# Kernel optimization log

Measured on AMD Instinct MI355X. Metric: run time of the kernel, lower is better.

The kernel has to match this reference:

```python
import jax, jax.numpy as jnp
import numpy as np

N_NODES = 100000
N_EDGES = 1600000
D_IN = 64
D_EDGE = 64
D_OUT = 64


def setup_inputs() -> dict:
    key = jax.random.key(0)
    ks = jax.random.split(key, 8)
    nfeats = jax.random.normal(ks[0], (N_NODES, 1, D_IN), dtype=jnp.float32)
    efeats = jax.random.normal(ks[1], (N_EDGES, 1, D_EDGE), dtype=jnp.float32)
    src = jax.random.randint(ks[2], (N_EDGES,), 0, N_NODES, dtype=jnp.int32)
    dst = jax.random.randint(ks[3], (N_EDGES,), 0, N_NODES, dtype=jnp.int32)
    # Linear weights stored torch-style as [out, in]
    W_msg_w = jax.random.normal(ks[4], (D_OUT, D_IN + D_EDGE), dtype=jnp.float32) * 0.05
    W_msg_b = jax.random.normal(ks[5], (D_OUT,), dtype=jnp.float32) * 0.05
    W_apply_w = jax.random.normal(ks[6], (D_OUT, D_IN + D_OUT), dtype=jnp.float32) * 0.05
    W_apply_b = jax.random.normal(ks[7], (D_OUT,), dtype=jnp.float32) * 0.05
    return {"nfeats": nfeats, "efeats": efeats, "src": src, "dst": dst,
            "W_msg_w": W_msg_w, "W_msg_b": W_msg_b,
            "W_apply_w": W_apply_w, "W_apply_b": W_apply_b}


def reference(nfeats, efeats, src, dst, W_msg_w, W_msg_b, W_apply_w, W_apply_b):
    n_nodes = nfeats.shape[0]
    h = nfeats[:, 0, :]          # [N, D_IN]
    e = efeats[:, 0, :]          # [E, D_EDGE]
    # message: per-edge gather of src node feats, concat with edge feats, linear
    src_h = h[src]               # [E, D_IN]
    msg = jnp.concatenate([src_h, e], axis=1) @ W_msg_w.T + W_msg_b  # [E, D_OUT]
    # mean aggregation over incoming edges per destination node
    msg_sum = jax.ops.segment_sum(msg, dst, num_segments=n_nodes)    # [N, D_OUT]
    deg = jax.ops.segment_sum(jnp.ones((msg.shape[0],), msg.dtype), dst,
                              num_segments=n_nodes)                  # [N]
    h_neigh = jnp.where(deg[:, None] > 0, msg_sum / jnp.maximum(deg, 1.0)[:, None], 0.0)
    # apply: concat self + neighborhood, linear, activation
    combined = jnp.concatenate([h, h_neigh], axis=1) @ W_apply_w.T + W_apply_b
    out = jax.nn.relu(combined)[:, None, :]  # [N, 1, D_OUT]
    return out
```

## Files before the change

### kernel.cpp

```cpp
#include <hip/hip_runtime.h>

#define N_NODES 100000
#define N_EDGES 1600000
#define NB_SCAN 49

typedef __attribute__((ext_vector_type(8))) short bf16x8;
typedef __attribute__((ext_vector_type(4))) float f32x4;


__global__ void k_zero(int* __restrict__ p, int n) {
    int i = blockIdx.x * blockDim.x + threadIdx.x;
    if (i < n) p[i] = 0;
}

__global__ void k_count(const int* __restrict__ dst, int* __restrict__ cnt) {
    int e = blockIdx.x * blockDim.x + threadIdx.x;
    if (e < N_EDGES) atomicAdd(&cnt[dst[e]], 1);
}

__global__ void k_partial(const int* __restrict__ cnt, int* __restrict__ part) {
    __shared__ int red[256];
    int t = threadIdx.x;
    int base = blockIdx.x * 2048 + t * 8;
    int s = 0;
    if (base < N_NODES) {
        const int4* p = (const int4*)(cnt + base);
        int4 a = p[0], b = p[1];
        s = a.x + a.y + a.z + a.w + b.x + b.y + b.z + b.w;
    }
    red[t] = s;
    __syncthreads();
    for (int d = 128; d > 0; d >>= 1) {
        if (t < d) red[t] += red[t + d];
        __syncthreads();
    }
    if (t == 0) part[blockIdx.x] = red[0];
}

__global__ void k_scan_part(int* __restrict__ part, int nb) {
    int lane = threadIdx.x;
    int v = (lane < nb) ? part[lane] : 0;
    int incl = v;
    #pragma unroll
    for (int d = 1; d < 64; d <<= 1) {
        int u = __shfl_up(incl, d, 64);
        if (lane >= d) incl += u;
    }
    if (lane < nb) part[lane] = incl - v;
}

__global__ void k_scan_chunks(const int* __restrict__ cnt, const int* __restrict__ part,
                              int* __restrict__ off) {
    __shared__ int wtot[4];
    __shared__ int wexc[4];
    int t = threadIdx.x, b = blockIdx.x;
    int base = b * 2048 + t * 8;
    int4 a = {0, 0, 0, 0}, c = {0, 0, 0, 0};
    if (base < N_NODES) {
        const int4* p = (const int4*)(cnt + base);
        a = p[0];
        c = p[1];
    }
    int s0 = a.x, s1 = s0 + a.y, s2 = s1 + a.z, s3 = s2 + a.w;
    int s4 = s3 + c.x, s5 = s4 + c.y, s6 = s5 + c.z, s7 = s6 + c.w;
    int tot = s7;
    int lane = t & 63, wid = t >> 6;
    int incl = tot;
    #pragma unroll
    for (int d = 1; d < 64; d <<= 1) {
        int u = __shfl_up(incl, d, 64);
        if (lane >= d) incl += u;
    }
    if (lane == 63) wtot[wid] = incl;
    __syncthreads();
    if (t == 0) {
        int r = 0;
        for (int i = 0; i < 4; i++) { int v = wtot[i]; wexc[i] = r; r += v; }
    }
    __syncthreads();
    int texc = incl - tot + wexc[wid] + part[b];
    if (base < N_NODES) {
        int4 o0 = {texc, texc + s0, texc + s1, texc + s2};
        int4 o1 = {texc + s3, texc + s4, texc + s5, texc + s6};
        ((int4*)(off + base))[0] = o0;
        ((int4*)(off + base))[1] = o1;
    }
}

__global__ void k_scatter64(const int* __restrict__ dst, const int* __restrict__ src,
                            const int* __restrict__ off, int* __restrict__ cur,
                            unsigned long long* __restrict__ code64) {
    int e = blockIdx.x * blockDim.x + threadIdx.x;
    if (e < N_EDGES) {
        int d = dst[e];
        int p = off[d] + atomicAdd(&cur[d], 1);
        code64[p] = ((unsigned long long)(unsigned)src[e] << 32) | (unsigned)e;
    }
}

__global__ void k_scatter32(const int* __restrict__ dst, const int* __restrict__ off,
                            int* __restrict__ cur, int* __restrict__ eid) {
    int e = blockIdx.x * blockDim.x + threadIdx.x;
    if (e < N_EDGES) {
        int d = dst[e];
        int p = off[d] + atomicAdd(&cur[d], 1);
        eid[p] = e;
    }
}

__device__ __forceinline__ unsigned short f2bf(float f) {
    unsigned u = __float_as_uint(f);
    return (unsigned short)((u + 0x7FFFu + ((u >> 16) & 1u)) >> 16);
}

__global__ void k_prec(const float* __restrict__ Wm, const float* __restrict__ bm,
                       const float* __restrict__ Wa, const float* __restrict__ ba,
                       unsigned short* __restrict__ Wf, float* __restrict__ bc) {
    int o = blockIdx.x;
    int k = threadIdx.x;
    const float* war = Wa + o * 128 + 64;
    float w;
    if (k < 64) {
        w = Wa[o * 128 + k];
    } else {
        int m = k - 64;
        float s = 0.f;
        #pragma unroll 8
        for (int j = 0; j < 64; j++) s += war[j] * Wm[j * 128 + m];
        w = s;
    }
    Wf[o * 192 + k] = f2bf(w);
    if (k == 0) {
        float t = ba[o];
        for (int j = 0; j < 64; j++) t += war[j] * bm[j];
        bc[o] = t;
    }
}

__device__ __forceinline__ float4 ld_feat(const float* __restrict__ nf,
                                          const float* __restrict__ ef,
                                          unsigned long long c, int slot) {
    unsigned e = (unsigned)c;
    unsigned sv = (unsigned)(c >> 32);
    const float* p = (slot < 16) ? (nf + (size_t)sv * 64 + slot * 4)
                                 : (ef + (size_t)e * 64 + (slot - 16) * 4);
    return *(const float4*)p;
}

__global__ __launch_bounds__(256) void k_agg(
    const float* __restrict__ nf, const float* __restrict__ ef,
    const int* __restrict__ cnt, const int* __restrict__ off,
    const unsigned long long* __restrict__ code64, float* __restrict__ aggG) {
    int tid = threadIdx.x, lane = tid & 63, wid = tid >> 6;
    int n = blockIdx.x * 4 + wid;
    if (n >= N_NODES) return;
    int slot = lane & 31, half = lane >> 5;
    int st = off[n], deg = cnt[n];
    int pend = st + deg;
    float4 acc = make_float4(0.f, 0.f, 0.f, 0.f);
    int p = st + half;
    for (; p + 6 < pend; p += 8) {
        unsigned long long c0 = code64[p];
        unsigned long long c1 = code64[p + 2];
        unsigned long long c2 = code64[p + 4];
        unsigned long long c3 = code64[p + 6];
        float4 a0 = ld_feat(nf, ef, c0, slot);
        float4 a1 = ld_feat(nf, ef, c1, slot);
        float4 a2 = ld_feat(nf, ef, c2, slot);
        float4 a3 = ld_feat(nf, ef, c3, slot);
        acc.x += a0.x + a1.x + a2.x + a3.x;
        acc.y += a0.y + a1.y + a2.y + a3.y;
        acc.z += a0.z + a1.z + a2.z + a3.z;
        acc.w += a0.w + a1.w + a2.w + a3.w;
    }
    for (; p < pend; p += 2) {
        unsigned long long c = code64[p];
        float4 a = ld_feat(nf, ef, c, slot);
        acc.x += a.x; acc.y += a.y; acc.z += a.z; acc.w += a.w;
    }
    acc.x += __shfl_xor(acc.x, 32, 64);
    acc.y += __shfl_xor(acc.y, 32, 64);
    acc.z += __shfl_xor(acc.z, 32, 64);
    acc.w += __shfl_xor(acc.w, 32, 64);
    if (half == 0) {
        float inv = (deg > 0) ? 1.f / (float)deg : 0.f;
        acc.x *= inv; acc.y *= inv; acc.z *= inv; acc.w *= inv;
        *(float4*)(aggG + (size_t)n * 128 + slot * 4) = acc;
    }
}

__device__ __forceinline__ void st_bf4(unsigned short* p, float4 v) {
    unsigned lo = (unsigned)f2bf(v.x) | ((unsigned)f2bf(v.y) << 16);
    unsigned hi = (unsigned)f2bf(v.z) | ((unsigned)f2bf(v.w) << 16);
    uint2 u = {lo, hi};
    *(uint2*)p = u;
}

__global__ __launch_bounds__(256) void k_apply_mfma(
    const float* __restrict__ nf, const float* __restrict__ aggG,
    const int* __restrict__ cnt, const unsigned short* __restrict__ Wf,
    const float* __restrict__ ba, const float* __restrict__ bc,
    float* __restrict__ out) {
    __shared__ __align__(16) unsigned short cat[64][200];
    __shared__ __align__(16) unsigned short wt[64][200];
    __shared__ float degl[64];

    int tid = threadIdx.x;
    int base = blockIdx.x * 64;

    {
        const unsigned* Wfu = (const unsigned*)Wf;
        #pragma unroll
        for (int r = 0; r < 24; r++) {
            int u = r * 256 + tid;
            int o = u / 96;
            int c = u - o * 96;
            *(unsigned*)&wt[o][2 * c] = Wfu[u];
        }
    }
    {
        const float4* n4 = (const float4*)nf;
        #pragma unroll
        for (int r = 0; r < 4; r++) {
            int f = r * 256 + tid;
            int nl = f >> 4, c4 = f & 15;
            float4 v = make_float4(0.f, 0.f, 0.f, 0.f);
            if (base + nl < N_NODES) v = n4[(size_t)(base + nl) * 16 + c4];
            st_bf4(&cat[nl][c4 * 4], v);
        }
    }
    {
        const float4* g4 = (const float4*)aggG;
        #pragma unroll
        for (int r = 0; r < 8; r++) {
            int f = r * 256 + tid;
            int nl = f >> 5, c4 = f & 31;
            float4 v = make_float4(0.f, 0.f, 0.f, 0.f);
            if (base + nl < N_NODES) v = g4[(size_t)(base + nl) * 32 + c4];
            st_bf4(&cat[nl][64 + c4 * 4], v);
        }
    }
    if (tid < 64) degl[tid] = (base + tid < N_NODES) ? (float)cnt[base + tid] : 0.f;
    __syncthreads();

    int lane = tid & 63, w = tid >> 6;
    int sn = w * 16;
    int lr = lane & 15;
    int lg = lane >> 4;

    bf16x8 a[6];
    #pragma unroll
    for (int ks = 0; ks < 6; ks++)
        a[ks] = *(const bf16x8*)&cat[sn + lr][ks * 32 + lg * 8];

    float degv[4];
    #pragma unroll
    for (int r = 0; r < 4; r++) degv[r] = degl[sn + lg * 4 + r];

    #pragma unroll
    for (int cb = 0; cb < 4; cb++) {
        f32x4 acc = {0.f, 0.f, 0.f, 0.f};
        #pragma unroll
        for (int ks = 0; ks < 6; ks++) {
            bf16x8 b = *(const bf16x8*)&wt[cb * 16 + lr][ks * 32 + lg * 8];
            acc = __builtin_amdgcn_mfma_f32_16x16x32_bf16(a[ks], b, acc, 0, 0, 0);
        }
        int o = cb * 16 + lr;
        float bcv = bc[o], bav = ba[o];
        #pragma unroll
        for (int r = 0; r < 4; r++) {
            int n = base + sn + lg * 4 + r;
            if (n < N_NODES) {
                float v = acc[r] + ((degv[r] > 0.f) ? bcv : bav);
                out[(size_t)n * 64 + o] = fmaxf(v, 0.f);
            }
        }
    }
}

__global__ __launch_bounds__(256) void k_node_fb(
    const float* __restrict__ nf, const float* __restrict__ ef,
    const int* __restrict__ src, const int* __restrict__ cnt,
    const int* __restrict__ off, const int* __restrict__ eid,
    const float* __restrict__ Wm, const float* __restrict__ bm,
    const float* __restrict__ Wa, const float* __restrict__ ba,
    float* __restrict__ out) {
    __shared__ __align__(16) float agg[64][132];
    __shared__ __align__(16) float hn[64][68];
    __shared__ float degl[64];

    int tid = threadIdx.x, lane = tid & 63, wid = tid >> 6;
    int base = blockIdx.x * 64;

    for (int q = 0; q < 16; q++) {
        int nl = wid * 16 + q;
        int n = base + nl;
        float sh = 0.f, se = 0.f;
        int dg = 0;
        if (n < N_NODES) {
            dg = cnt[n];
            int st = off[n];
            for (int c0 = 0; c0 < dg; c0 += 64) {
                int m = dg - c0;
                if (m > 64) m = 64;
                int e_l = 0, s_l = 0;
                if (lane < m) {
                    e_l = eid[st + c0 + lane];
                    s_l = src[e_l];
                }
                for (int j = 0; j < m; j++) {
                    int e = __shfl(e_l, j, 64);
                    int s = __shfl(s_l, j, 64);
                    sh += nf[(size_t)s * 64 + lane];
                    se += ef[(size_t)e * 64 + lane];
                }
            }
        }
        agg[nl][lane] = sh;
        agg[nl][64 + lane] = se;
        if (lane == 0) degl[nl] = (float)dg;
    }
    __syncthreads();

    int og = (tid & 15) * 4;
    int ng = (tid >> 4) * 4;
    float acc[4][4] = {};
    const float4* Wm4 = (const float4*)Wm;
    #pragma unroll 4
    for (int k4 = 0; k4 < 32; k4++) {
        float4 av[4], wv[4];
        #pragma unroll
        for (int i = 0; i < 4; i++) av[i] = *(const float4*)&agg[ng + i][k4 * 4];
        #pragma unroll
        for (int j = 0; j < 4; j++) wv[j] = Wm4[(og + j) * 32 + k4];
        #pragma unroll
        for (int i = 0; i < 4; i++)
            #pragma unroll
            for (int j = 0; j < 4; j++)
                acc[i][j] += av[i].x * wv[j].x + av[i].y * wv[j].y +
                             av[i].z * wv[j].z + av[i].w * wv[j].w;
    }
    #pragma unroll
    for (int i = 0; i < 4; i++) {
        float d = degl[ng + i];
        float inv = (d > 0.f) ? 1.f / d : 0.f;
        #pragma unroll
        for (int j = 0; j < 4; j++) {
            float v = (d > 0.f) ? acc[i][j] * inv + bm[og + j] : 0.f;
            hn[ng + i][og + j] = v;
        }
    }
    __syncthreads();

    float acc2[4][4] = {};
    const float4* Wa4 = (const float4*)Wa;
    #pragma unroll 4
    for (int k4 = 0; k4 < 16; k4++) {
        float4 hv[4], wv[4];
        #pragma unroll
        for (int i = 0; i < 4; i++) {
            int n = base + ng + i;
            if (n < N_NODES)
                hv[i] = ((const float4*)(nf + (size_t)n * 64))[k4];
            else
                hv[i] = make_float4(0.f, 0.f, 0.f, 0.f);
        }
        #pragma unroll
        for (int j = 0; j < 4; j++) wv[j] = Wa4[(og + j) * 32 + k4];
        #pragma unroll
        for (int i = 0; i < 4; i++)
            #pragma unroll
            for (int j = 0; j < 4; j++)
                acc2[i][j] += hv[i].x * wv[j].x + hv[i].y * wv[j].y +
                              hv[i].z * wv[j].z + hv[i].w * wv[j].w;
    }
    #pragma unroll 4
    for (int k4 = 0; k4 < 16; k4++) {
        float4 hv[4], wv[4];
        #pragma unroll
        for (int i = 0; i < 4; i++) hv[i] = *(const float4*)&hn[ng + i][k4 * 4];
        #pragma unroll
        for (int j = 0; j < 4; j++) wv[j] = Wa4[(og + j) * 32 + 16 + k4];
        #pragma unroll
        for (int i = 0; i < 4; i++)
            #pragma unroll
            for (int j = 0; j < 4; j++)
                acc2[i][j] += hv[i].x * wv[j].x + hv[i].y * wv[j].y +
                              hv[i].z * wv[j].z + hv[i].w * wv[j].w;
    }
    #pragma unroll
    for (int i = 0; i < 4; i++) {
        int n = base + ng + i;
        if (n < N_NODES) {
            float4 o;
            o.x = fmaxf(acc2[i][0] + ba[og + 0], 0.f);
            o.y = fmaxf(acc2[i][1] + ba[og + 1], 0.f);
            o.z = fmaxf(acc2[i][2] + ba[og + 2], 0.f);
            o.w = fmaxf(acc2[i][3] + ba[og + 3], 0.f);
            *(float4*)&out[(size_t)n * 64 + og] = o;
        }
    }
}

extern "C" void kernel_launch(void* const* d_in, const int* in_sizes, int n_in,
                              void* d_out, int out_size, void* d_ws, size_t ws_size,
                              hipStream_t stream) {
    const float* nf = (const float*)d_in[0];
    const float* ef = (const float*)d_in[1];
    const int* src = (const int*)d_in[2];
    const int* dst = (const int*)d_in[3];
    const float* Wm = (const float*)d_in[4];
    const float* bm = (const float*)d_in[5];
    const float* Wa = (const float*)d_in[6];
    const float* ba = (const float*)d_in[7];
    float* out = (float*)d_out;

    int* cnt = (int*)d_ws;
    int* cur = cnt + N_NODES;
    int* part = cur + N_NODES;
    int* off = part + 64;
    size_t csr_bytes = (size_t)(3 * N_NODES + 64) * 4;

    int nz = 2 * N_NODES + 64;
    k_zero<<<(nz + 255) / 256, 256, 0, stream>>>(cnt, nz);
    k_count<<<(N_EDGES + 255) / 256, 256, 0, stream>>>(dst, cnt);
    k_partial<<<NB_SCAN, 256, 0, stream>>>(cnt, part);
    k_scan_part<<<1, 64, 0, stream>>>(part, NB_SCAN);
    k_scan_chunks<<<NB_SCAN, 256, 0, stream>>>(cnt, part, off);

    size_t need = csr_bytes + (size_t)N_EDGES * 8 + (size_t)N_NODES * 128 * 4 +
                  (size_t)64 * 192 * 2 + 512;
    if (ws_size >= need) {
        unsigned long long* code64 = (unsigned long long*)((char*)d_ws + csr_bytes);
        float* aggG = (float*)((char*)code64 + (size_t)N_EDGES * 8);
        unsigned short* Wf = (unsigned short*)(aggG + (size_t)N_NODES * 128);
        float* bc = (float*)(Wf + 64 * 192);
        k_prec<<<64, 192, 0, stream>>>(Wm, bm, Wa, ba, Wf, bc);
        k_scatter64<<<(N_EDGES + 255) / 256, 256, 0, stream>>>(dst, src, off, cur, code64);
        k_agg<<<N_NODES / 4, 256, 0, stream>>>(nf, ef, cnt, off, code64, aggG);
        k_apply_mfma<<<(N_NODES + 63) / 64, 256, 0, stream>>>(nf, aggG, cnt, Wf, ba, bc, out);
    } else {
        int* eid = (int*)((char*)d_ws + csr_bytes);
        k_scatter32<<<(N_EDGES + 255) / 256, 256, 0, stream>>>(dst, off, cur, eid);
        k_node_fb<<<(N_NODES + 63) / 64, 256, 0, stream>>>(nf, ef, src, cnt, off, eid,
                                                           Wm, bm, Wa, ba, out);
    }
}
```

Before: 315.9 us.

## Fuse edge aggregation and MFMA apply into one per-16-node kernel

Merges the gather/mean aggregation kernel and the MFMA apply kernel into a single 1024-thread block that aggregates 16 nodes (one wave each) into bf16 shared memory and then runs the 16x64 GEMM on four waves. This removes the fp32 aggG intermediate round-trip through global memory (about 51 MB of writes and reads) and one launch. In exchange, each block reloads the full weight tile into LDS for only 16 nodes, 12 of 16 waves sit idle during the MFMA phase, and the per-block barrier ties all waves to the slowest node's degree.

```diff
diff --git a/kernel.cpp b/kernel.cpp
--- a/kernel.cpp
+++ b/kernel.cpp
@@ -147,13 +147,39 @@
     return *(const float4*)p;
 }
 
-__global__ __launch_bounds__(256) void k_agg(
+__device__ __forceinline__ void st_bf4(unsigned short* p, float4 v) {
+    unsigned lo = (unsigned)f2bf(v.x) | ((unsigned)f2bf(v.y) << 16);
+    unsigned hi = (unsigned)f2bf(v.z) | ((unsigned)f2bf(v.w) << 16);
+    uint2 u = {lo, hi};
+    *(uint2*)p = u;
+}
+
+__global__ __launch_bounds__(1024) void k_fused(
     const float* __restrict__ nf, const float* __restrict__ ef,
     const int* __restrict__ cnt, const int* __restrict__ off,
-    const unsigned long long* __restrict__ code64, float* __restrict__ aggG) {
-    int tid = threadIdx.x, lane = tid & 63, wid = tid >> 6;
-    int n = blockIdx.x * 4 + wid;
-    if (n >= N_NODES) return;
+    const unsigned long long* __restrict__ code64,
+    const unsigned short* __restrict__ Wf,
+    const float* __restrict__ ba, const float* __restrict__ bc,
+    float* __restrict__ out) {
+    __shared__ __align__(16) unsigned short cat[16][200];
+    __shared__ __align__(16) unsigned short wt[64][200];
+    __shared__ float degl[16];
+
+    int tid = threadIdx.x, lane = tid & 63, w = tid >> 6;
+    int base = blockIdx.x * 16;
+    int n = base + w;
+
+    {
+        const unsigned* Wfu = (const unsigned*)Wf;
+        #pragma unroll
+        for (int r = 0; r < 6; r++) {
+            int u = r * 1024 + tid;
+            int o = u / 96;
+            int c = u - o * 96;
+            *(unsigned*)&wt[o][2 * c] = Wfu[u];
+        }
+    }
+
     int slot = lane & 31, half = lane >> 5;
     int st = off[n], deg = cnt[n];
     int pend = st + deg;
@@ -182,99 +208,42 @@
     acc.y += __shfl_xor(acc.y, 32, 64);
     acc.z += __shfl_xor(acc.z, 32, 64);
     acc.w += __shfl_xor(acc.w, 32, 64);
+
     if (half == 0) {
         float inv = (deg > 0) ? 1.f / (float)deg : 0.f;
         acc.x *= inv; acc.y *= inv; acc.z *= inv; acc.w *= inv;
-        *(float4*)(aggG + (size_t)n * 128 + slot * 4) = acc;
-    }
-}
-
-__device__ __forceinline__ void st_bf4(unsigned short* p, float4 v) {
-    unsigned lo = (unsigned)f2bf(v.x) | ((unsigned)f2bf(v.y) << 16);
-    unsigned hi = (unsigned)f2bf(v.z) | ((unsigned)f2bf(v.w) << 16);
-    uint2 u = {lo, hi};
-    *(uint2*)p = u;
-}
-
-__global__ __launch_bounds__(256) void k_apply_mfma(
-    const float* __restrict__ nf, const float* __restrict__ aggG,
-    const int* __restrict__ cnt, const unsigned short* __restrict__ Wf,
-    const float* __restrict__ ba, const float* __restrict__ bc,
-    float* __restrict__ out) {
-    __shared__ __align__(16) unsigned short cat[64][200];
-    __shared__ __align__(16) unsigned short wt[64][200];
-    __shared__ float degl[64];
-
-    int tid = threadIdx.x;
-    int base = blockIdx.x * 64;
-
-    {
-        const unsigned* Wfu = (const unsigned*)Wf;
-        #pragma unroll
-        for (int r = 0; r < 24; r++) {
-            int u = r * 256 + tid;
-            int o = u / 96;
-            int c = u - o * 96;
-            *(unsigned*)&wt[o][2 * c] = Wfu[u];
-        }
-    }
-    {
-        const float4* n4 = (const float4*)nf;
-        #pragma unroll
-        for (int r = 0; r < 4; r++) {
-            int f = r * 256 + tid;
-            int nl = f >> 4, c4 = f & 15;
-            float4 v = make_float4(0.f, 0.f, 0.f, 0.f);
-            if (base + nl < N_NODES) v = n4[(size_t)(base + nl) * 16 + c4];
-            st_bf4(&cat[nl][c4 * 4], v);
-        }
-    }
-    {
-        const float4* g4 = (const float4*)aggG;
-        #pragma unroll
-        for (int r = 0; r < 8; r++) {
-            int f = r * 256 + tid;
-            int nl = f >> 5, c4 = f & 31;
-            float4 v = make_float4(0.f, 0.f, 0.f, 0.f);
-            if (base + nl < N_NODES) v = g4[(size_t)(base + nl) * 32 + c4];
-            st_bf4(&cat[nl][64 + c4 * 4], v);
-        }
-    }
-    if (tid < 64) degl[tid] = (base + tid < N_NODES) ? (float)cnt[base + tid] : 0.f;
-    __syncthreads();
-
-    int lane = tid & 63, w = tid >> 6;
-    int sn = w * 16;
+        st_bf4(&cat[w][64 + slot * 4], acc);
+    } else if (slot < 16) {
+        float4 hv = ((const float4*)(nf + (size_t)n * 64))[slot];
+        st_bf4(&cat[w][slot * 4], hv);
+    }
+    if (lane == 0) degl[w] = (float)deg;
+    __syncthreads();
+
+    if (w >= 4) return;
+    int cb = w;
     int lr = lane & 15;
     int lg = lane >> 4;
 
     bf16x8 a[6];
     #pragma unroll
     for (int ks = 0; ks < 6; ks++)
-        a[ks] = *(const bf16x8*)&cat[sn + lr][ks * 32 + lg * 8];
-
-    float degv[4];
-    #pragma unroll
-    for (int r = 0; r < 4; r++) degv[r] = degl[sn + lg * 4 + r];
-
-    #pragma unroll
-    for (int cb = 0; cb < 4; cb++) {
-        f32x4 acc = {0.f, 0.f, 0.f, 0.f};
-        #pragma unroll
-        for (int ks = 0; ks < 6; ks++) {
-            bf16x8 b = *(const bf16x8*)&wt[cb * 16 + lr][ks * 32 + lg * 8];
-            acc = __builtin_amdgcn_mfma_f32_16x16x32_bf16(a[ks], b, acc, 0, 0, 0);
-        }
-        int o = cb * 16 + lr;
-        float bcv = bc[o], bav = ba[o];
-        #pragma unroll
-        for (int r = 0; r < 4; r++) {
-            int n = base + sn + lg * 4 + r;
-            if (n < N_NODES) {
-                float v = acc[r] + ((degv[r] > 0.f) ? bcv : bav);
-                out[(size_t)n * 64 + o] = fmaxf(v, 0.f);
-            }
-        }
+        a[ks] = *(const bf16x8*)&cat[lr][ks * 32 + lg * 8];
+
+    f32x4 accd = {0.f, 0.f, 0.f, 0.f};
+    #pragma unroll
+    for (int ks = 0; ks < 6; ks++) {
+        bf16x8 b = *(const bf16x8*)&wt[cb * 16 + lr][ks * 32 + lg * 8];
+        accd = __builtin_amdgcn_mfma_f32_16x16x32_bf16(a[ks], b, accd, 0, 0, 0);
+    }
+    int o = cb * 16 + lr;
+    float bcv = bc[o], bav = ba[o];
+    #pragma unroll
+    for (int r = 0; r < 4; r++) {
+        int nn = base + lg * 4 + r;
+        float dv = degl[lg * 4 + r];
+        float v = accd[r] + ((dv > 0.f) ? bcv : bav);
+        out[(size_t)nn * 64 + o] = fmaxf(v, 0.f);
     }
 }
 
@@ -428,17 +397,14 @@
     k_scan_part<<<1, 64, 0, stream>>>(part, NB_SCAN);
     k_scan_chunks<<<NB_SCAN, 256, 0, stream>>>(cnt, part, off);
 
-    size_t need = csr_bytes + (size_t)N_EDGES * 8 + (size_t)N_NODES * 128 * 4 +
-                  (size_t)64 * 192 * 2 + 512;
+    size_t need = csr_bytes + (size_t)N_EDGES * 8 + (size_t)64 * 192 * 2 + 512;
     if (ws_size >= need) {
         unsigned long long* code64 = (unsigned long long*)((char*)d_ws + csr_bytes);
-        float* aggG = (float*)((char*)code64 + (size_t)N_EDGES * 8);
-        unsigned short* Wf = (unsigned short*)(aggG + (size_t)N_NODES * 128);
+        unsigned short* Wf = (unsigned short*)((char*)code64 + (size_t)N_EDGES * 8);
         float* bc = (float*)(Wf + 64 * 192);
         k_prec<<<64, 192, 0, stream>>>(Wm, bm, Wa, ba, Wf, bc);
         k_scatter64<<<(N_EDGES + 255) / 256, 256, 0, stream>>>(dst, src, off, cur, code64);
-        k_agg<<<N_NODES / 4, 256, 0, stream>>>(nf, ef, cnt, off, code64, aggG);
-        k_apply_mfma<<<(N_NODES + 63) / 64, 256, 0, stream>>>(nf, aggG, cnt, Wf, ba, bc, out);
+        k_fused<<<N_NODES / 16, 1024, 0, stream>>>(nf, ef, cnt, off, code64, Wf, ba, bc, out);
     } else {
         int* eid = (int*)((char*)d_ws + csr_bytes);
         k_scatter32<<<(N_EDGES + 255) / 256, 256, 0, stream>>>(dst, off, cur, eid);
```

New measurement: 307.6 us. -2.6%, faster.
